# Optimization experiments

Measured on AMD Instinct MI355X. Metric: run time of the kernel, lower is better.

Reference implementation:

```python
import jax, jax.numpy as jnp
import numpy as np

N_QUBITS = 6

def _apply_1q(state, U, w):
    # state: [B] + [2]*6 complex; U: [2,2] complex
    ax = 1 + w
    s = jnp.moveaxis(state, ax, -1)
    s = jnp.einsum('...j,ij->...i', s, U)
    return jnp.moveaxis(s, -1, ax)

def _apply_cnot(state, ctrl, tgt):
    ca, ta = 1 + ctrl, 1 + tgt
    s = jnp.moveaxis(state, (ca, ta), (1, 2))  # [B,2,2,...]
    s = jnp.stack([s[:, 0], s[:, 1, ::-1]], axis=1)
    return jnp.moveaxis(s, (1, 2), (ca, ta))

def _rot(phi, theta, omega):
    # PennyLane Rot = RZ(omega) RY(theta) RZ(phi)
    c, s = jnp.cos(theta / 2), jnp.sin(theta / 2)
    return jnp.stack([
        jnp.stack([jnp.exp(-0.5j * (phi + omega)) * c, -jnp.exp(0.5j * (phi - omega)) * s]),
        jnp.stack([jnp.exp(-0.5j * (phi - omega)) * s, jnp.exp(0.5j * (phi + omega)) * c]),
    ])

def _quantum(xq, qw):
    B = xq.shape[0]
    # AngleEmbedding RY: product state, per-qubit amplitudes [cos(x/2), sin(x/2)]
    amps = jnp.stack([jnp.cos(xq / 2), jnp.sin(xq / 2)], axis=-1)  # [B,6,2]
    state = amps[:, 0]
    for i in range(1, N_QUBITS):
        state = jnp.einsum('b...,bj->b...j', state, amps[:, i])
    state = state.astype(jnp.complex64)  # [B,2,2,2,2,2,2]
    # StronglyEntanglingLayers: per layer Rot on each wire, then CNOT ring of range r
    n_layers = qw.shape[0]
    for l in range(n_layers):
        for w in range(N_QUBITS):
            U = _rot(qw[l, w, 0], qw[l, w, 1], qw[l, w, 2])
            state = _apply_1q(state, U, w)
        r = (l % (N_QUBITS - 1)) + 1  # default ranges
        for w in range(N_QUBITS):
            state = _apply_cnot(state, w, (w + r) % N_QUBITS)
    probs = jnp.abs(state) ** 2
    zs = []
    for w in range(N_QUBITS):
        axes = tuple(a for a in range(1, N_QUBITS + 1) if a != 1 + w)
        p = jnp.sum(probs, axis=axes)  # [B,2]
        zs.append(p[:, 0] - p[:, 1])
    return jnp.stack(zs, axis=-1)  # [B,6]

def setup_inputs() -> dict:
    key = jax.random.key(0)
    ks = jax.random.split(key, 10)
    B = 16384
    return {
        'xc': jax.random.normal(ks[0], (B, 2048), jnp.float32),
        'xq': jax.random.uniform(ks[1], (B, N_QUBITS), jnp.float32),
        'W1': jax.random.normal(ks[2], (64, 2048), jnp.float32) * 0.02,
        'b1': jnp.zeros((64,), jnp.float32),
        'qw': jax.random.uniform(ks[3], (3, N_QUBITS, 3), jnp.float32, 0.0, 2 * np.pi),
        'Wq': jax.random.normal(ks[4], (16, N_QUBITS), jnp.float32) * 0.3,
        'bq': jnp.zeros((16,), jnp.float32),
        'Wf': jax.random.normal(ks[5], (3, 80), jnp.float32) * 0.1,
        'bf': jnp.zeros((3,), jnp.float32),
    }

def reference(xc, xq, W1, b1, qw, Wq, bq, Wf, bf):
    c = jax.nn.relu(xc @ W1.T + b1)                 # [B,64]
    q = _quantum(xq, qw) @ Wq.T + bq                # [B,16]
    return jnp.concatenate([c, q], axis=1) @ Wf.T + bf  # [B,3]
```

## Files before the change

kernel.cpp:

```cpp
#include <hip/hip_runtime.h>
#include <hip/hip_bf16.h>

#define NQ 6

typedef __attribute__((ext_vector_type(8))) short short8;
typedef __attribute__((ext_vector_type(4))) float floatx4;

#define WS_MQ_F   8192
#define WS_CQ_F   (8192+18)
#define WS_W1BF_B 36864

__global__ __launch_bounds__(64) void prep_kernel(
    const float* __restrict__ qw, int n_layers,
    const float* __restrict__ W1, const float* __restrict__ Wq,
    const float* __restrict__ bq, const float* __restrict__ Wf,
    const float* __restrict__ bf, float* __restrict__ ws_f,
    short* __restrict__ w1bf)
{
    const int blk  = blockIdx.x;
    const int lane = threadIdx.x;

    if (blk == 0) {
        if (lane < 18) {
            int j = lane / 6, wi = lane % 6;
            float s = 0.f;
            for (int m = 0; m < 16; ++m) s += Wf[j*80 + 64 + m] * Wq[m*6 + wi];
            ws_f[WS_MQ_F + lane] = s;
        } else if (lane < 21) {
            int j = lane - 18;
            float s = bf[j];
            for (int m = 0; m < 16; ++m) s += Wf[j*80 + 64 + m] * bq[m];
            ws_f[WS_CQ_F + j] = s;
        }
    } else if (blk <= 64) {
        const int j = blk - 1;
        float re = (lane == j) ? 1.f : 0.f;
        float im = 0.f;
        for (int l = 0; l < n_layers; ++l) {
            for (int w = 0; w < NQ; ++w) {
                const float* g = qw + (l*NQ + w)*3;
                float phi = g[0], th = g[1], om = g[2];
                float c, s;  __sincosf(0.5f*th, &s, &c);
                float sa, ca; __sincosf(0.5f*(phi+om), &sa, &ca);
                float sb, cb; __sincosf(0.5f*(phi-om), &sb, &cb);
                float u00r =  c*ca, u00i = -c*sa;
                float u01r = -s*cb, u01i = -s*sb;
                float u10r =  s*cb, u10i = -s*sb;
                float u11r =  c*ca, u11i =  c*sa;
                int p = 5 - w, mask = 1 << p;
                float pre = __shfl_xor(re, mask, 64);
                float pim = __shfl_xor(im, mask, 64);
                int b = (lane >> p) & 1;
                float mr = b ? u11r : u00r, mi = b ? u11i : u00i;
                float pr = b ? u10r : u01r, pi = b ? u10i : u01i;
                float nre = mr*re - mi*im + pr*pre - pi*pim;
                float nim = mr*im + mi*re + pr*pim + pi*pre;
                re = nre; im = nim;
            }
            int r = l % (NQ-1) + 1;
            for (int w = 0; w < NQ; ++w) {
                int tgt = (w + r) % NQ;
                int tmask = 1 << (5 - tgt);
                float pre = __shfl_xor(re, tmask, 64);
                float pim = __shfl_xor(im, tmask, 64);
                int cs = (lane >> (5 - w)) & 1;
                re = cs ? pre : re;
                im = cs ? pim : im;
            }
        }
        ws_f[(lane*64 + j)*2 + 0] = re;
        ws_f[(lane*64 + j)*2 + 1] = im;
    } else {
        int idx = (blk - 65)*512 + lane*8;
        if (idx < 64*2048) {
            float4 a0 = *(const float4*)(W1 + idx);
            float4 a1 = *(const float4*)(W1 + idx + 4);
            union { short8 v; __hip_bfloat162 h[4]; } u;
            float2 f;
            f.x=a0.x; f.y=a0.y; u.h[0] = __float22bfloat162_rn(f);
            f.x=a0.z; f.y=a0.w; u.h[1] = __float22bfloat162_rn(f);
            f.x=a1.x; f.y=a1.y; u.h[2] = __float22bfloat162_rn(f);
            f.x=a1.z; f.y=a1.w; u.h[3] = __float22bfloat162_rn(f);
            *(short8*)(w1bf + idx) = u.v;
        }
    }
}

__global__ __launch_bounds__(1024) void fused_kernel(
    const float* __restrict__ xq, const float2* __restrict__ U,
    const float* __restrict__ ws_f,
    const float* __restrict__ xc, const short* __restrict__ w1bf,
    const float* __restrict__ b1, const float* __restrict__ Wf,
    float* __restrict__ out)
{
    const int tid  = threadIdx.x;
    const int lane = tid & 63;
    const int t    = __builtin_amdgcn_readfirstlane((int)(tid >> 6));
    const int blk  = blockIdx.x;

    __shared__ float zbuf[16][64][6];
    __shared__ float qres[64][3];
    __shared__ float cl[64][65];

    {
        const int b = blk*64 + lane;
        const float* x = xq + (size_t)b*6;
        float ah[8], al[8];
        ah[0] = 1.f;
        #pragma unroll
        for (int q = 0; q < 3; ++q) {
            float c, s; __sincosf(0.5f*x[q], &s, &c);
            const int sz = 1 << q;
            #pragma unroll
            for (int m = sz-1; m >= 0; --m) {
                float v = ah[m];
                ah[2*m+1] = v*s;
                ah[2*m+0] = v*c;
            }
        }
        al[0] = 1.f;
        #pragma unroll
        for (int q = 0; q < 3; ++q) {
            float c, s; __sincosf(0.5f*x[3+q], &s, &c);
            const int sz = 1 << q;
            #pragma unroll
            for (int m = sz-1; m >= 0; --m) {
                float v = al[m];
                al[2*m+1] = v*s;
                al[2*m+0] = v*c;
            }
        }

        float zp[6] = {0,0,0,0,0,0};
        const float2* Urow = U + t*4*64;
        for (int ii = 0; ii < 4; ++ii) {
            float rr = 0.f, ri = 0.f;
            #pragma unroll
            for (int jh = 0; jh < 8; ++jh) {
                float sr = 0.f, si = 0.f;
                #pragma unroll
                for (int jl = 0; jl < 8; ++jl) {
                    float2 u = Urow[ii*64 + jh*8 + jl];
                    sr += u.x * al[jl];
                    si += u.y * al[jl];
                }
                rr += ah[jh] * sr;
                ri += ah[jh] * si;
            }
            float p = rr*rr + ri*ri;
            int i = t*4 + ii;
            #pragma unroll
            for (int w = 0; w < 6; ++w) zp[w] += ((i >> (5-w)) & 1) ? -p : p;
        }
        #pragma unroll
        for (int w = 0; w < 6; ++w) zbuf[t][lane][w] = zp[w];
    }
    __syncthreads();
    if (t == 0) {
        float z[6];
        #pragma unroll
        for (int w = 0; w < 6; ++w) {
            float s = 0.f;
            #pragma unroll
            for (int sbi = 0; sbi < 16; ++sbi) s += zbuf[sbi][lane][w];
            z[w] = s;
        }
        #pragma unroll
        for (int j = 0; j < 3; ++j) {
            float v = ws_f[WS_CQ_F + j];
            #pragma unroll
            for (int w = 0; w < 6; ++w) v += ws_f[WS_MQ_F + j*6 + w] * z[w];
            qres[lane][j] = v;
        }
    }

    const int wr = t >> 2, wc = t & 3;
    const int row  = blk*64 + wr*16 + (lane & 15);
    const int koff = (lane >> 4) * 8;

    const float* ap = xc + (size_t)row*2048 + koff;
    const short* bp = w1bf + (wc*16 + (lane & 15))*2048 + koff;

    floatx4 acc = {0,0,0,0};

    float4 a0 = *(const float4*)ap;
    float4 a1 = *(const float4*)(ap + 4);
    short8 bv = *(const short8*)bp;

    #pragma unroll 4
    for (int kk = 1; kk < 64; ++kk) {
        float4 na0 = *(const float4*)(ap + kk*32);
        float4 na1 = *(const float4*)(ap + kk*32 + 4);
        short8 nbv = *(const short8*)(bp + kk*32);

        union { short8 v; __hip_bfloat162 h[4]; } af;
        float2 f;
        f.x=a0.x; f.y=a0.y; af.h[0] = __float22bfloat162_rn(f);
        f.x=a0.z; f.y=a0.w; af.h[1] = __float22bfloat162_rn(f);
        f.x=a1.x; f.y=a1.y; af.h[2] = __float22bfloat162_rn(f);
        f.x=a1.z; f.y=a1.w; af.h[3] = __float22bfloat162_rn(f);

        acc = __builtin_amdgcn_mfma_f32_16x16x32_bf16(af.v, bv, acc, 0, 0, 0);

        a0 = na0; a1 = na1; bv = nbv;
    }
    {
        union { short8 v; __hip_bfloat162 h[4]; } af;
        float2 f;
        f.x=a0.x; f.y=a0.y; af.h[0] = __float22bfloat162_rn(f);
        f.x=a0.z; f.y=a0.w; af.h[1] = __float22bfloat162_rn(f);
        f.x=a1.x; f.y=a1.y; af.h[2] = __float22bfloat162_rn(f);
        f.x=a1.z; f.y=a1.w; af.h[3] = __float22bfloat162_rn(f);
        acc = __builtin_amdgcn_mfma_f32_16x16x32_bf16(af.v, bv, acc, 0, 0, 0);
    }

    const int rbase = wr*16 + ((lane >> 4) * 4);
    const int c0 = wc*16 + (lane & 15);
    const float bb = b1[c0];
    #pragma unroll
    for (int r = 0; r < 4; ++r)
        cl[rbase + r][c0] = fmaxf(acc[r] + bb, 0.f);
    __syncthreads();

    const int rr2 = tid & 63;
    if (t < 3) {
        float v = 0.f;
        #pragma unroll
        for (int col = 0; col < 64; ++col) v += Wf[t*80 + col] * cl[rr2][col];
        int g = blk*64 + rr2;
        out[(size_t)g*3 + t] = v + qres[rr2][t];
    }
}

extern "C" void kernel_launch(void* const* d_in, const int* in_sizes, int n_in,
                              void* d_out, int out_size, void* d_ws, size_t ws_size,
                              hipStream_t stream) {
    const float* xc = (const float*)d_in[0];
    const float* xq = (const float*)d_in[1];
    const float* W1 = (const float*)d_in[2];
    const float* b1 = (const float*)d_in[3];
    const float* qw = (const float*)d_in[4];
    const float* Wq = (const float*)d_in[5];
    const float* bq = (const float*)d_in[6];
    const float* Wf = (const float*)d_in[7];
    const float* bf = (const float*)d_in[8];
    float* out = (float*)d_out;

    const int B = in_sizes[1] / NQ;
    const int n_layers = in_sizes[4] / (NQ * 3);

    char* ws = (char*)d_ws;
    float*  ws_f  = (float*)ws;
    float2* U     = (float2*)ws;
    short*  w1bf  = (short*)(ws + WS_W1BF_B);

    prep_kernel<<<dim3(321), dim3(64), 0, stream>>>(qw, n_layers, W1, Wq, bq, Wf, bf, ws_f, w1bf);
    fused_kernel<<<dim3(B/64), dim3(1024), 0, stream>>>(xq, U, ws_f, xc, w1bf, b1, Wf, out);
}
```

Measured before the change: 259.0 us.

## Stage xc tiles through double-buffered swizzled LDS and prefetch before quantum phase

Each block now cooperatively loads its 64x2048 xc rows once per 128-wide K chunk, converts them to bf16 and stores them in a double-buffered, XOR-swizzled LDS tile. Each wave then reads its A fragments from LDS, so the four column waves no longer each reload the same xc rows from global memory. The first xc and W1 chunks are loaded before the quantum simulation to hide latency. In exchange the kernel adds a block-wide barrier per chunk and 32KB of LDS.

```diff
diff --git a/kernel.cpp b/kernel.cpp
--- a/kernel.cpp
+++ b/kernel.cpp
@@ -86,6 +86,16 @@
     }
 }
 
+__device__ __forceinline__ short8 cvt_bf16x8(float4 a0, float4 a1) {
+    union { short8 v; __hip_bfloat162 h[4]; } u;
+    float2 f;
+    f.x=a0.x; f.y=a0.y; u.h[0] = __float22bfloat162_rn(f);
+    f.x=a0.z; f.y=a0.w; u.h[1] = __float22bfloat162_rn(f);
+    f.x=a1.x; f.y=a1.y; u.h[2] = __float22bfloat162_rn(f);
+    f.x=a1.z; f.y=a1.w; u.h[3] = __float22bfloat162_rn(f);
+    return u.v;
+}
+
 __global__ __launch_bounds__(1024) void fused_kernel(
     const float* __restrict__ xq, const float2* __restrict__ U,
     const float* __restrict__ ws_f,
@@ -98,18 +108,44 @@
     const int t    = __builtin_amdgcn_readfirstlane((int)(tid >> 6));
     const int blk  = blockIdx.x;
 
+    __shared__ __align__(16) short Abuf[2][64*128];
     __shared__ float zbuf[16][64][6];
     __shared__ float qres[64][3];
     __shared__ float cl[64][65];
 
+    const int wr = t >> 2, wc = t & 3;
+    const int srow = tid >> 4;
+    const int sgrp = tid & 15;
+    const float* asrc = xc + (size_t)(blk*64 + srow)*2048 + sgrp*8;
+    const int adoff = srow*128 + ((sgrp ^ (srow & 7)) << 3);
+    const int arow = wr*16 + (lane & 15);
+    const int abase = arow*128;
+    const int arx = arow & 7;
+    const int a_l = lane >> 4;
+    const short* bp = w1bf + (wc*16 + (lane & 15))*2048 + a_l*8;
+
+    const float* xrow = xq + (size_t)(blk*64 + lane)*6;
+    float2 xq01 = *(const float2*)(xrow);
+    float2 xq23 = *(const float2*)(xrow + 2);
+    float2 xq45 = *(const float2*)(xrow + 4);
+
+    float4 sA0[2], sA1[2];
+    sA0[0] = *(const float4*)(asrc + 0*128);
+    sA1[0] = *(const float4*)(asrc + 0*128 + 4);
+    sA0[1] = *(const float4*)(asrc + 1*128);
+    sA1[1] = *(const float4*)(asrc + 1*128 + 4);
+    short8 bv0 = *(const short8*)(bp + 0);
+    short8 bv1 = *(const short8*)(bp + 32);
+    short8 bv2 = *(const short8*)(bp + 64);
+    short8 bv3 = *(const short8*)(bp + 96);
+
     {
-        const int b = blk*64 + lane;
-        const float* x = xq + (size_t)b*6;
+        const float xs[6] = {xq01.x, xq01.y, xq23.x, xq23.y, xq45.x, xq45.y};
         float ah[8], al[8];
         ah[0] = 1.f;
         #pragma unroll
         for (int q = 0; q < 3; ++q) {
-            float c, s; __sincosf(0.5f*x[q], &s, &c);
+            float c, s; __sincosf(0.5f*xs[q], &s, &c);
             const int sz = 1 << q;
             #pragma unroll
             for (int m = sz-1; m >= 0; --m) {
@@ -121,7 +157,7 @@
         al[0] = 1.f;
         #pragma unroll
         for (int q = 0; q < 3; ++q) {
-            float c, s; __sincosf(0.5f*x[3+q], &s, &c);
+            float c, s; __sincosf(0.5f*xs[3+q], &s, &c);
             const int sz = 1 << q;
             #pragma unroll
             for (int m = sz-1; m >= 0; --m) {
@@ -174,47 +210,45 @@
         }
     }
 
-    const int wr = t >> 2, wc = t & 3;
-    const int row  = blk*64 + wr*16 + (lane & 15);
-    const int koff = (lane >> 4) * 8;
-
-    const float* ap = xc + (size_t)row*2048 + koff;
-    const short* bp = w1bf + (wc*16 + (lane & 15))*2048 + koff;
+    *(short8*)(&Abuf[0][adoff]) = cvt_bf16x8(sA0[0], sA1[0]);
+    __syncthreads();
 
     floatx4 acc = {0,0,0,0};
 
-    float4 a0 = *(const float4*)ap;
-    float4 a1 = *(const float4*)(ap + 4);
-    short8 bv = *(const short8*)bp;
-
-    #pragma unroll 4
-    for (int kk = 1; kk < 64; ++kk) {
-        float4 na0 = *(const float4*)(ap + kk*32);
-        float4 na1 = *(const float4*)(ap + kk*32 + 4);
-        short8 nbv = *(const short8*)(bp + kk*32);
-
-        union { short8 v; __hip_bfloat162 h[4]; } af;
-        float2 f;
-        f.x=a0.x; f.y=a0.y; af.h[0] = __float22bfloat162_rn(f);
-        f.x=a0.z; f.y=a0.w; af.h[1] = __float22bfloat162_rn(f);
-        f.x=a1.x; f.y=a1.y; af.h[2] = __float22bfloat162_rn(f);
-        f.x=a1.z; f.y=a1.w; af.h[3] = __float22bfloat162_rn(f);
-
-        acc = __builtin_amdgcn_mfma_f32_16x16x32_bf16(af.v, bv, acc, 0, 0, 0);
-
-        a0 = na0; a1 = na1; bv = nbv;
-    }
-    {
-        union { short8 v; __hip_bfloat162 h[4]; } af;
-        float2 f;
-        f.x=a0.x; f.y=a0.y; af.h[0] = __float22bfloat162_rn(f);
-        f.x=a0.z; f.y=a0.w; af.h[1] = __float22bfloat162_rn(f);
-        f.x=a1.x; f.y=a1.y; af.h[2] = __float22bfloat162_rn(f);
-        f.x=a1.z; f.y=a1.w; af.h[3] = __float22bfloat162_rn(f);
-        acc = __builtin_amdgcn_mfma_f32_16x16x32_bf16(af.v, bv, acc, 0, 0, 0);
-    }
-
-    const int rbase = wr*16 + ((lane >> 4) * 4);
+    #pragma unroll
+    for (int c = 0; c < 16; ++c) {
+        const int cb = c & 1;
+
+        if (c + 2 < 16) {
+            sA0[cb] = *(const float4*)(asrc + (c+2)*128);
+            sA1[cb] = *(const float4*)(asrc + (c+2)*128 + 4);
+        }
+        short8 nb0, nb1, nb2, nb3;
+        if (c + 1 < 16) {
+            nb0 = *(const short8*)(bp + (c+1)*128 + 0);
+            nb1 = *(const short8*)(bp + (c+1)*128 + 32);
+            nb2 = *(const short8*)(bp + (c+1)*128 + 64);
+            nb3 = *(const short8*)(bp + (c+1)*128 + 96);
+        }
+
+        const short* abp = &Abuf[cb][abase];
+        short8 av0 = *(const short8*)(abp + ((((0*4 + a_l)) ^ arx) << 3));
+        short8 av1 = *(const short8*)(abp + ((((1*4 + a_l)) ^ arx) << 3));
+        short8 av2 = *(const short8*)(abp + ((((2*4 + a_l)) ^ arx) << 3));
+        short8 av3 = *(const short8*)(abp + ((((3*4 + a_l)) ^ arx) << 3));
+        acc = __builtin_amdgcn_mfma_f32_16x16x32_bf16(av0, bv0, acc, 0, 0, 0);
+        acc = __builtin_amdgcn_mfma_f32_16x16x32_bf16(av1, bv1, acc, 0, 0, 0);
+        acc = __builtin_amdgcn_mfma_f32_16x16x32_bf16(av2, bv2, acc, 0, 0, 0);
+        acc = __builtin_amdgcn_mfma_f32_16x16x32_bf16(av3, bv3, acc, 0, 0, 0);
+
+        if (c + 1 < 16) {
+            *(short8*)(&Abuf[cb ^ 1][adoff]) = cvt_bf16x8(sA0[cb ^ 1], sA1[cb ^ 1]);
+            bv0 = nb0; bv1 = nb1; bv2 = nb2; bv3 = nb3;
+            __syncthreads();
+        }
+    }
+
+    const int rbase = wr*16 + (a_l * 4);
     const int c0 = wc*16 + (lane & 15);
     const float bb = b1[c0];
     #pragma unroll
```

Result: faster. 219.7 us (-15.2%).

## Split quantum part into separate kernel and restructure GEMM with split-K tiles

Applied to the files above, without the earlier changes.

Moves the quantum simulation into its own kernel that writes per-row results to workspace. The GEMM kernel now handles 16 rows per 256-thread block: each wave covers a quarter of K for all 64 output columns using four MFMA accumulators, and partial sums are reduced through shared memory. This aims to remove the large 1024-thread block with its heavy shared-memory footprint and to raise occupancy and the number of blocks for streaming xc. The cost is an extra kernel launch, a global round trip for the quantum results, and a shared-memory reduction.

```diff
diff --git a/kernel.cpp b/kernel.cpp
--- a/kernel.cpp
+++ b/kernel.cpp
@@ -9,6 +9,7 @@
 #define WS_MQ_F   8192
 #define WS_CQ_F   (8192+18)
 #define WS_W1BF_B 36864
+#define WS_QPART_B 301056
 
 __global__ __launch_bounds__(64) void prep_kernel(
     const float* __restrict__ qw, int n_layers,
@@ -86,149 +87,180 @@
     }
 }
 
-__global__ __launch_bounds__(1024) void fused_kernel(
+__device__ __forceinline__ short8 cvt_bf16x8(float4 a0, float4 a1) {
+    union { short8 v; __hip_bfloat162 h[4]; } u;
+    float2 f;
+    f.x=a0.x; f.y=a0.y; u.h[0] = __float22bfloat162_rn(f);
+    f.x=a0.z; f.y=a0.w; u.h[1] = __float22bfloat162_rn(f);
+    f.x=a1.x; f.y=a1.y; u.h[2] = __float22bfloat162_rn(f);
+    f.x=a1.z; f.y=a1.w; u.h[3] = __float22bfloat162_rn(f);
+    return u.v;
+}
+
+__global__ __launch_bounds__(256) void qpart_kernel(
     const float* __restrict__ xq, const float2* __restrict__ U,
-    const float* __restrict__ ws_f,
+    const float* __restrict__ ws_f, float* __restrict__ qpart)
+{
+    const int lane = threadIdx.x & 63;
+    const int t = __builtin_amdgcn_readfirstlane((int)(threadIdx.x >> 6));
+    const int b = blockIdx.x*64 + lane;
+
+    __shared__ float zbuf[4][64][6];
+
+    const float* x = xq + (size_t)b*6;
+    float ah[8], al[8];
+    ah[0] = 1.f;
+    #pragma unroll
+    for (int q = 0; q < 3; ++q) {
+        float c, s; __sincosf(0.5f*x[q], &s, &c);
+        const int sz = 1 << q;
+        #pragma unroll
+        for (int m = sz-1; m >= 0; --m) {
+            float v = ah[m];
+            ah[2*m+1] = v*s;
+            ah[2*m+0] = v*c;
+        }
+    }
+    al[0] = 1.f;
+    #pragma unroll
+    for (int q = 0; q < 3; ++q) {
+        float c, s; __sincosf(0.5f*x[3+q], &s, &c);
+        const int sz = 1 << q;
+        #pragma unroll
+        for (int m = sz-1; m >= 0; --m) {
+            float v = al[m];
+            al[2*m+1] = v*s;
+            al[2*m+0] = v*c;
+        }
+    }
+
+    float zp[6] = {0,0,0,0,0,0};
+    const float2* Urow = U + t*16*64;
+    for (int ii = 0; ii < 16; ++ii) {
+        float rr = 0.f, ri = 0.f;
+        #pragma unroll
+        for (int jh = 0; jh < 8; ++jh) {
+            float sr = 0.f, si = 0.f;
+            #pragma unroll
+            for (int jl = 0; jl < 8; ++jl) {
+                float2 u = Urow[ii*64 + jh*8 + jl];
+                sr += u.x * al[jl];
+                si += u.y * al[jl];
+            }
+            rr += ah[jh] * sr;
+            ri += ah[jh] * si;
+        }
+        float p = rr*rr + ri*ri;
+        int i = t*16 + ii;
+        #pragma unroll
+        for (int w = 0; w < 6; ++w) zp[w] += ((i >> (5-w)) & 1) ? -p : p;
+    }
+    #pragma unroll
+    for (int w = 0; w < 6; ++w) zbuf[t][lane][w] = zp[w];
+    __syncthreads();
+    if (t == 0) {
+        float z[6];
+        #pragma unroll
+        for (int w = 0; w < 6; ++w)
+            z[w] = zbuf[0][lane][w] + zbuf[1][lane][w] + zbuf[2][lane][w] + zbuf[3][lane][w];
+        #pragma unroll
+        for (int j = 0; j < 3; ++j) {
+            float v = ws_f[WS_CQ_F + j];
+            #pragma unroll
+            for (int w = 0; w < 6; ++w) v += ws_f[WS_MQ_F + j*6 + w] * z[w];
+            qpart[(size_t)b*3 + j] = v;
+        }
+    }
+}
+
+__global__ __launch_bounds__(256, 4) void gemm_kernel(
     const float* __restrict__ xc, const short* __restrict__ w1bf,
     const float* __restrict__ b1, const float* __restrict__ Wf,
-    float* __restrict__ out)
+    const float* __restrict__ qpart, float* __restrict__ out)
 {
     const int tid  = threadIdx.x;
     const int lane = tid & 63;
     const int t    = __builtin_amdgcn_readfirstlane((int)(tid >> 6));
     const int blk  = blockIdx.x;
-
-    __shared__ float zbuf[16][64][6];
-    __shared__ float qres[64][3];
-    __shared__ float cl[64][65];
-
+    const int rb   = blk * 16;
+
+    __shared__ float accbuf[4][64][20];
+    __shared__ float cl[16][65];
+
+    const int a_l = lane >> 4;
+    const int m16 = lane & 15;
+
+    const float* ap = xc + (size_t)(rb + m16)*2048 + t*512 + a_l*8;
+    const short* bp = w1bf + m16*2048 + t*512 + a_l*8;
+
+    floatx4 acc0 = {0,0,0,0}, acc1 = {0,0,0,0}, acc2 = {0,0,0,0}, acc3 = {0,0,0,0};
+
+    float4 a0  = *(const float4*)ap;
+    float4 a1  = *(const float4*)(ap + 4);
+    short8 b0  = *(const short8*)(bp);
+    short8 bv1 = *(const short8*)(bp + 16*2048);
+    short8 b2  = *(const short8*)(bp + 32*2048);
+    short8 b3  = *(const short8*)(bp + 48*2048);
+
+    #pragma unroll
+    for (int s = 1; s < 16; ++s) {
+        const float* apn = ap + s*32;
+        const short* bpn = bp + s*32;
+        float4 na0 = *(const float4*)apn;
+        float4 na1 = *(const float4*)(apn + 4);
+        short8 nb0 = *(const short8*)(bpn);
+        short8 nb1 = *(const short8*)(bpn + 16*2048);
+        short8 nb2 = *(const short8*)(bpn + 32*2048);
+        short8 nb3 = *(const short8*)(bpn + 48*2048);
+
+        short8 av = cvt_bf16x8(a0, a1);
+        acc0 = __builtin_amdgcn_mfma_f32_16x16x32_bf16(av, b0,  acc0, 0, 0, 0);
+        acc1 = __builtin_amdgcn_mfma_f32_16x16x32_bf16(av, bv1, acc1, 0, 0, 0);
+        acc2 = __builtin_amdgcn_mfma_f32_16x16x32_bf16(av, b2,  acc2, 0, 0, 0);
+        acc3 = __builtin_amdgcn_mfma_f32_16x16x32_bf16(av, b3,  acc3, 0, 0, 0);
+
+        a0 = na0; a1 = na1; b0 = nb0; bv1 = nb1; b2 = nb2; b3 = nb3;
+    }
     {
-        const int b = blk*64 + lane;
-        const float* x = xq + (size_t)b*6;
-        float ah[8], al[8];
-        ah[0] = 1.f;
-        #pragma unroll
-        for (int q = 0; q < 3; ++q) {
-            float c, s; __sincosf(0.5f*x[q], &s, &c);
-            const int sz = 1 << q;
-            #pragma unroll
-            for (int m = sz-1; m >= 0; --m) {
-                float v = ah[m];
-                ah[2*m+1] = v*s;
-                ah[2*m+0] = v*c;
-            }
-        }
-        al[0] = 1.f;
-        #pragma unroll
-        for (int q = 0; q < 3; ++q) {
-            float c, s; __sincosf(0.5f*x[3+q], &s, &c);
-            const int sz = 1 << q;
-            #pragma unroll
-            for (int m = sz-1; m >= 0; --m) {
-                float v = al[m];
-                al[2*m+1] = v*s;
-                al[2*m+0] = v*c;
-            }
-        }
-
-        float zp[6] = {0,0,0,0,0,0};
-        const float2* Urow = U + t*4*64;
-        for (int ii = 0; ii < 4; ++ii) {
-            float rr = 0.f, ri = 0.f;
-            #pragma unroll
-            for (int jh = 0; jh < 8; ++jh) {
-                float sr = 0.f, si = 0.f;
-                #pragma unroll
-                for (int jl = 0; jl < 8; ++jl) {
-                    float2 u = Urow[ii*64 + jh*8 + jl];
-                    sr += u.x * al[jl];
-                    si += u.y * al[jl];
-                }
-                rr += ah[jh] * sr;
-                ri += ah[jh] * si;
-            }
-            float p = rr*rr + ri*ri;
-            int i = t*4 + ii;
-            #pragma unroll
-            for (int w = 0; w < 6; ++w) zp[w] += ((i >> (5-w)) & 1) ? -p : p;
-        }
-        #pragma unroll
-        for (int w = 0; w < 6; ++w) zbuf[t][lane][w] = zp[w];
+        short8 av = cvt_bf16x8(a0, a1);
+        acc0 = __builtin_amdgcn_mfma_f32_16x16x32_bf16(av, b0,  acc0, 0, 0, 0);
+        acc1 = __builtin_amdgcn_mfma_f32_16x16x32_bf16(av, bv1, acc1, 0, 0, 0);
+        acc2 = __builtin_amdgcn_mfma_f32_16x16x32_bf16(av, b2,  acc2, 0, 0, 0);
+        acc3 = __builtin_amdgcn_mfma_f32_16x16x32_bf16(av, b3,  acc3, 0, 0, 0);
+    }
+
+    #pragma unroll
+    for (int r = 0; r < 4; ++r) {
+        accbuf[t][lane][ 0 + r] = acc0[r];
+        accbuf[t][lane][ 4 + r] = acc1[r];
+        accbuf[t][lane][ 8 + r] = acc2[r];
+        accbuf[t][lane][12 + r] = acc3[r];
     }
     __syncthreads();
-    if (t == 0) {
-        float z[6];
-        #pragma unroll
-        for (int w = 0; w < 6; ++w) {
-            float s = 0.f;
-            #pragma unroll
-            for (int sbi = 0; sbi < 16; ++sbi) s += zbuf[sbi][lane][w];
-            z[w] = s;
-        }
-        #pragma unroll
-        for (int j = 0; j < 3; ++j) {
-            float v = ws_f[WS_CQ_F + j];
-            #pragma unroll
-            for (int w = 0; w < 6; ++w) v += ws_f[WS_MQ_F + j*6 + w] * z[w];
-            qres[lane][j] = v;
-        }
-    }
-
-    const int wr = t >> 2, wc = t & 3;
-    const int row  = blk*64 + wr*16 + (lane & 15);
-    const int koff = (lane >> 4) * 8;
-
-    const float* ap = xc + (size_t)row*2048 + koff;
-    const short* bp = w1bf + (wc*16 + (lane & 15))*2048 + koff;
-
-    floatx4 acc = {0,0,0,0};
-
-    float4 a0 = *(const float4*)ap;
-    float4 a1 = *(const float4*)(ap + 4);
-    short8 bv = *(const short8*)bp;
-
-    #pragma unroll 4
-    for (int kk = 1; kk < 64; ++kk) {
-        float4 na0 = *(const float4*)(ap + kk*32);
-        float4 na1 = *(const float4*)(ap + kk*32 + 4);
-        short8 nbv = *(const short8*)(bp + kk*32);
-
-        union { short8 v; __hip_bfloat162 h[4]; } af;
-        float2 f;
-        f.x=a0.x; f.y=a0.y; af.h[0] = __float22bfloat162_rn(f);
-        f.x=a0.z; f.y=a0.w; af.h[1] = __float22bfloat162_rn(f);
-        f.x=a1.x; f.y=a1.y; af.h[2] = __float22bfloat162_rn(f);
-        f.x=a1.z; f.y=a1.w; af.h[3] = __float22bfloat162_rn(f);
-
-        acc = __builtin_amdgcn_mfma_f32_16x16x32_bf16(af.v, bv, acc, 0, 0, 0);
-
-        a0 = na0; a1 = na1; bv = nbv;
-    }
+
     {
-        union { short8 v; __hip_bfloat162 h[4]; } af;
-        float2 f;
-        f.x=a0.x; f.y=a0.y; af.h[0] = __float22bfloat162_rn(f);
-        f.x=a0.z; f.y=a0.w; af.h[1] = __float22bfloat162_rn(f);
-        f.x=a1.x; f.y=a1.y; af.h[2] = __float22bfloat162_rn(f);
-        f.x=a1.z; f.y=a1.w; af.h[3] = __float22bfloat162_rn(f);
-        acc = __builtin_amdgcn_mfma_f32_16x16x32_bf16(af.v, bv, acc, 0, 0, 0);
-    }
-
-    const int rbase = wr*16 + ((lane >> 4) * 4);
-    const int c0 = wc*16 + (lane & 15);
-    const float bb = b1[c0];
-    #pragma unroll
-    for (int r = 0; r < 4; ++r)
-        cl[rbase + r][c0] = fmaxf(acc[r] + bb, 0.f);
+        const int m  = tid & 15;
+        const int nb4 = tid >> 4;
+        #pragma unroll
+        for (int q = 0; q < 4; ++q) {
+            const int n = nb4*4 + q;
+            const int lsrc = (m >> 2)*16 + (n & 15);
+            const int reg  = (n >> 4)*4 + (m & 3);
+            float v = accbuf[0][lsrc][reg] + accbuf[1][lsrc][reg]
+                    + accbuf[2][lsrc][reg] + accbuf[3][lsrc][reg];
+            cl[m][n] = fmaxf(v + b1[n], 0.f);
+        }
+    }
     __syncthreads();
 
-    const int rr2 = tid & 63;
-    if (t < 3) {
+    if (tid < 48) {
+        const int j = tid >> 4;
+        const int m = tid & 15;
         float v = 0.f;
         #pragma unroll
-        for (int col = 0; col < 64; ++col) v += Wf[t*80 + col] * cl[rr2][col];
-        int g = blk*64 + rr2;
-        out[(size_t)g*3 + t] = v + qres[rr2][t];
+        for (int col = 0; col < 64; ++col) v += Wf[j*80 + col] * cl[m][col];
+        const int g = rb + m;
+        out[(size_t)g*3 + j] = v + qpart[(size_t)g*3 + j];
     }
 }
 
@@ -253,7 +285,9 @@
     float*  ws_f  = (float*)ws;
     float2* U     = (float2*)ws;
     short*  w1bf  = (short*)(ws + WS_W1BF_B);
+    float*  qpart = (float*)(ws + WS_QPART_B);
 
     prep_kernel<<<dim3(321), dim3(64), 0, stream>>>(qw, n_layers, W1, Wq, bq, Wf, bf, ws_f, w1bf);
-    fused_kernel<<<dim3(B/64), dim3(1024), 0, stream>>>(xq, U, ws_f, xc, w1bf, b1, Wf, out);
-}
+    qpart_kernel<<<dim3(B/64), dim3(256), 0, stream>>>(xq, U, ws_f, qpart);
+    gemm_kernel<<<dim3(B/16), dim3(256), 0, stream>>>(xc, w1bf, b1, Wf, qpart, out);
+}
```

Result: faster. 248.4 us (-4.1%).
